# Kernel tuning notes

Hardware: AMD Instinct MI355X
Metric: run time of the kernel (lower is better)

## Reference

```python
import jax, jax.numpy as jnp
import numpy as np

EMBED_DIM = 1024
NUM_HEADS = 16
HEAD_DIM = EMBED_DIM // NUM_HEADS


def setup_inputs() -> dict:
    key = jax.random.key(0)
    k1, k2, k3, k4 = jax.random.split(key, 4)
    B, N, C = 4, 4096, EMBED_DIM
    x = jax.random.normal(k1, (B, N, C), dtype=jnp.float32)
    scale = 1.0 / np.sqrt(C)
    W_qkv = jax.random.normal(k2, (C, 3 * C), dtype=jnp.float32) * scale
    W_out = jax.random.normal(k3, (C, C), dtype=jnp.float32) * scale
    b_out = jax.random.normal(k4, (C,), dtype=jnp.float32) * 0.01
    return {"x": x, "W_qkv": W_qkv, "W_out": W_out, "b_out": b_out}


def reference(x, W_qkv, W_out, b_out):
    B, N, C = x.shape
    H, D = NUM_HEADS, HEAD_DIM
    qkv = (x @ W_qkv).reshape(B, N, 3, H, D)
    qkv = jnp.transpose(qkv, (2, 0, 3, 1, 4))  # (3, B, H, N, D)
    q, k, v = qkv[0], qkv[1], qkv[2]
    q = jax.nn.elu(q) + 1.0
    k = jax.nn.elu(k) + 1.0
    kv = jnp.einsum('bhnd,bhne->bhde', k, v)          # (B,H,D,D)
    num = jnp.einsum('bhnd,bhde->bhne', q, kv)        # (B,H,N,D)
    normalizer = jnp.einsum('bhnd,bhd->bhn', q, k.sum(axis=2))
    out = num / (normalizer[..., None] + 1e-6)
    out = jnp.transpose(out, (0, 2, 1, 3)).reshape(B, N, C)
    return out @ W_out + b_out
```

## Files before the change

kernel.cpp:

```cpp
#include <hip/hip_runtime.h>
#include <hip/hip_bf16.h>

using bf16x8 = __bf16 __attribute__((ext_vector_type(8)));
using f32x4  = float  __attribute__((ext_vector_type(4)));
using u16x8  = unsigned short __attribute__((ext_vector_type(8)));
using u16x4  = unsigned short __attribute__((ext_vector_type(4)));

__device__ __forceinline__ unsigned short f2bf(float f) {
  unsigned u = __builtin_bit_cast(unsigned, f);
  u += 0x7fffu + ((u >> 16) & 1u);
  return (unsigned short)(u >> 16);
}
__device__ __forceinline__ float bf2f(unsigned short h) {
  return __builtin_bit_cast(float, (unsigned)h << 16);
}

__device__ __forceinline__ void gload16(const void* g, void* l) {
  __builtin_amdgcn_global_load_lds(
      (const __attribute__((address_space(1))) void*)g,
      (__attribute__((address_space(3))) void*)l, 16, 0, 0);
}

__device__ __forceinline__ void barrier_raw() {
  asm volatile("" ::: "memory");
  __builtin_amdgcn_s_barrier();
  asm volatile("" ::: "memory");
}
#define VMC4() asm volatile("s_waitcnt vmcnt(4)" ::: "memory")
#define VMC0() asm volatile("s_waitcnt vmcnt(0)" ::: "memory")
#define SGB(mask, n) __builtin_amdgcn_sched_group_barrier(mask, n, 0)

__global__ __launch_bounds__(256) void conv_f32_bf16(const float* __restrict__ in,
                                                     unsigned short* __restrict__ out, int n) {
  int stride = gridDim.x * 256 * 4;
  for (int i = (blockIdx.x * 256 + threadIdx.x) * 4; i < n; i += stride) {
    float4 v = *reinterpret_cast<const float4*>(in + i);
    u16x4 o = { f2bf(v.x), f2bf(v.y), f2bf(v.z), f2bf(v.w) };
    *reinterpret_cast<u16x4*>(out + i) = o;
  }
}

__global__ __launch_bounds__(256) void transpose_f32_bf16(const float* __restrict__ in,
                                                          unsigned short* __restrict__ out,
                                                          int R, int C) {
  __shared__ float t[64][65];
  int c0 = blockIdx.x * 64, r0 = blockIdx.y * 64;
  int lx = threadIdx.x & 63, ly = threadIdx.x >> 6;
#pragma unroll
  for (int i = 0; i < 16; ++i) {
    int r = ly * 16 + i;
    t[r][lx] = in[(size_t)(r0 + r) * C + c0 + lx];
  }
  __syncthreads();
#pragma unroll
  for (int i = 0; i < 16; ++i) {
    int c = ly * 16 + i;
    out[(size_t)(c0 + c) * R + r0 + lx] = f2bf(t[lx][c]);
  }
}

__device__ __forceinline__ void gemm256_mainloop(
    const unsigned short* __restrict__ A, const unsigned short* __restrict__ Bt,
    int brow, int bcol, char* lds, f32x4 (&acc)[8][4]) {
  constexpr int NT = 16;
  const int tid  = threadIdx.x;
  const int lane = tid & 63;
  const int w    = tid >> 6;
  const int wr   = w >> 2, wc = w & 3;
  const int lr   = lane & 15, kg = lane >> 4;

  const int o0 = tid * 16;
  const int p0 = o0 ^ (((o0 >> 7) & 7) << 4);
  const int off0 = (p0 >> 7) * 2048 + (p0 & 127);
  const int wq = w << 10;

  const int xr  = (lr & 7) << 4;
  const int ck0 = (kg * 16) ^ xr;
  const int aoff = wr * 16384 + lr * 128;
  const int boff = 32768 + (wc >> 1) * 16384 + (wc & 1) * 8192 + lr * 128;

  const char* rA00 = lds + aoff + ck0;
  const char* rA01 = lds + aoff + (ck0 ^ 64);
  const char* rA10 = rA00 + 65536;
  const char* rA11 = rA01 + 65536;
  const char* rB00 = lds + boff + ck0;
  const char* rB01 = lds + boff + (ck0 ^ 64);
  const char* rB10 = rB00 + 65536;
  const char* rB11 = rB01 + 65536;

  const char* gA0 = (const char*)(A  + (size_t)brow * 1024) + off0;
  const char* gA1 = (const char*)(A  + (size_t)(brow + 128) * 1024) + off0;
  const char* gB0 = (const char*)(Bt + (size_t)bcol * 1024) + off0;
  const char* gB1 = (const char*)(Bt + (size_t)(bcol + 128) * 1024) + off0;

  auto STG = [&](const char*& g, int region) {
    gload16(g, lds + region + wq);
    gload16(g + 131072, lds + region + 8192 + wq);
    g += 128;
  };

  bf16x8 aQ[4][2], aR[4][2], bL0[2][2], bL1[2][2], bH[2][2];

  auto READ_A = [&](bf16x8 (&dst)[4][2], const char* pk0, const char* pk1, int mb) {
#pragma unroll
    for (int m = 0; m < 4; ++m) {
      dst[m][0] = __builtin_bit_cast(bf16x8, *(const u16x8*)(pk0 + (mb + m) * 2048));
      dst[m][1] = __builtin_bit_cast(bf16x8, *(const u16x8*)(pk1 + (mb + m) * 2048));
    }
  };
  auto READ_B = [&](bf16x8 (&dst)[2][2], const char* pk0, const char* pk1, int nb) {
#pragma unroll
    for (int n = 0; n < 2; ++n) {
      dst[n][0] = __builtin_bit_cast(bf16x8, *(const u16x8*)(pk0 + (nb + n) * 2048));
      dst[n][1] = __builtin_bit_cast(bf16x8, *(const u16x8*)(pk1 + (nb + n) * 2048));
    }
  };
  auto MFMA_Q = [&](int mb, int nb, bf16x8 (&Af)[4][2], bf16x8 (&Bf)[2][2]) {
#pragma unroll
    for (int kk = 0; kk < 2; ++kk)
#pragma unroll
      for (int m = 0; m < 4; ++m)
#pragma unroll
        for (int n = 0; n < 2; ++n)
          acc[mb + m][nb + n] =
              __builtin_amdgcn_mfma_f32_16x16x32_bf16(Af[m][kk], Bf[n][kk], acc[mb + m][nb + n], 0, 0, 0);
  };
  auto INTERLEAVE_P123 = [&]() {
#pragma unroll
    for (int s = 0; s < 12; ++s) { SGB(0x100, 1); SGB(0x8, 4); }
  };

  STG(gB0, 32768); STG(gB1, 49152);
  STG(gA0, 0);     STG(gA1, 16384);
  STG(gB0, 65536 + 32768); STG(gB1, 65536 + 49152);
  VMC4();
  barrier_raw();
  READ_A(aQ, rA00, rA01, 0);
  READ_B(bL0, rB00, rB01, 0);
  __builtin_amdgcn_s_setprio(1);

  for (int t = 0; t < NT; t += 2) {
    if (t + 1 < NT) { STG(gA0, 65536); STG(gA1, 65536 + 16384); }
    READ_B(bH, rB00, rB01, 2);
    MFMA_Q(0, 0, aQ, bL0);
    READ_A(aR, rA00, rA01, 4);
    MFMA_Q(0, 2, aQ, bH);
    MFMA_Q(4, 2, aR, bH);
    INTERLEAVE_P123();
    __builtin_amdgcn_s_setprio(0);
    barrier_raw();
    if (t + 2 < NT) {
      STG(gB0, 32768); STG(gB1, 49152);
      VMC4();
    } else if (t + 1 < NT) {
      VMC0();
    }
    barrier_raw();
    __builtin_amdgcn_s_setprio(1);
    if (t + 1 < NT) { READ_A(aQ, rA10, rA11, 0); READ_B(bL1, rB10, rB11, 0); }
    MFMA_Q(4, 0, aR, bL0);

    if (t + 1 < NT) {
      if (t + 2 < NT) { STG(gA0, 0); STG(gA1, 16384); }
      READ_B(bH, rB10, rB11, 2);
      MFMA_Q(0, 0, aQ, bL1);
      READ_A(aR, rA10, rA11, 4);
      MFMA_Q(0, 2, aQ, bH);
      MFMA_Q(4, 2, aR, bH);
      INTERLEAVE_P123();
      __builtin_amdgcn_s_setprio(0);
      barrier_raw();
      if (t + 3 < NT) {
        STG(gB0, 65536 + 32768); STG(gB1, 65536 + 49152);
        VMC4();
      } else if (t + 2 < NT) {
        VMC0();
      }
      barrier_raw();
      __builtin_amdgcn_s_setprio(1);
      if (t + 2 < NT) { READ_A(aQ, rA00, rA01, 0); READ_B(bL0, rB00, rB01, 0); }
      MFMA_Q(4, 0, aR, bL1);
    }
  }
  __builtin_amdgcn_s_setprio(0);
}

__global__ __launch_bounds__(512, 2) void gemm_qkv(
    const unsigned short* __restrict__ xbf, const unsigned short* __restrict__ wt,
    unsigned short* __restrict__ q, unsigned short* __restrict__ k, unsigned short* __restrict__ v) {
  __shared__ __align__(16) char lds[131072];
  f32x4 acc[8][4] = {};
  const int bid = blockIdx.x;
  const int r = bid & 7, i = bid >> 3;
  const int tm = r * 8 + (i & 7);
  const int tn = i >> 3;
  const int brow = tm * 256, bcol = tn * 256;
  gemm256_mainloop(xbf, wt, brow, bcol, lds, acc);

  const int lane = threadIdx.x & 63, w = threadIdx.x >> 6;
  const int wr = w >> 2, wc = w & 3;
  const int lr = lane & 15, kg = lane >> 4;
#pragma unroll
  for (int m = 0; m < 8; ++m)
#pragma unroll
    for (int n = 0; n < 4; ++n)
#pragma unroll
      for (int rr = 0; rr < 4; ++rr) {
        int grow = brow + wr * 128 + m * 16 + kg * 4 + rr;
        int gcol = bcol + wc * 64 + n * 16 + lr;
        float val = acc[m][n][rr];
        int tt = gcol >> 10;
        int h = (gcol >> 6) & 15;
        int d = gcol & 63;
        int b = grow >> 12, s = grow & 4095;
        size_t idx = ((size_t)(b * 16 + h) * 4096 + s) * 64 + d;
        if (tt < 2) {
          val = val > 0.f ? val + 1.f : __expf(val);
          (tt == 0 ? q : k)[idx] = f2bf(val);
        } else {
          v[idx] = f2bf(val);
        }
      }
}

__global__ __launch_bounds__(512, 2) void gemm_out(
    const unsigned short* __restrict__ attn, const unsigned short* __restrict__ wt,
    const float* __restrict__ bias, float* __restrict__ out) {
  __shared__ __align__(16) char lds[131072];
  f32x4 acc[8][4] = {};
  const int bid = blockIdx.x;
  const int r = bid & 7, i = bid >> 3;
  const int tm = r * 8 + (i & 7);
  const int tn = i >> 3;
  const int brow = tm * 256, bcol = tn * 256;
  gemm256_mainloop(attn, wt, brow, bcol, lds, acc);

  const int lane = threadIdx.x & 63, w = threadIdx.x >> 6;
  const int wr = w >> 2, wc = w & 3;
  const int lr = lane & 15, kg = lane >> 4;
#pragma unroll
  for (int m = 0; m < 8; ++m)
#pragma unroll
    for (int n = 0; n < 4; ++n)
#pragma unroll
      for (int rr = 0; rr < 4; ++rr) {
        int grow = brow + wr * 128 + m * 16 + kg * 4 + rr;
        int gcol = bcol + wc * 64 + n * 16 + lr;
        out[(size_t)grow * 1024 + gcol] = acc[m][n][rr] + bias[gcol];
      }
}

__global__ __launch_bounds__(256) void kv_kernel(
    const unsigned short* __restrict__ k, const unsigned short* __restrict__ v,
    float* __restrict__ kv, float* __restrict__ ksum) {
  const int bid = blockIdx.x;
  const int bh = bid >> 3, chunk = bid & 7;
  const unsigned short* kb = k + (size_t)bh * 4096 * 64 + chunk * 512 * 64;
  const unsigned short* vb = v + (size_t)bh * 4096 * 64 + chunk * 512 * 64;
  __shared__ unsigned short ks[64 * 64];
  __shared__ unsigned short vs[64 * 64];
  const int tid = threadIdx.x;
  const int ty = tid >> 4, tx = tid & 15;
  float acc[4][4] = {};
  float ksacc[4] = {};
  for (int t = 0; t < 8; ++t) {
    const unsigned short* ksrc = kb + t * 4096;
    const unsigned short* vsrc = vb + t * 4096;
    *reinterpret_cast<u16x8*>(&ks[tid * 8])        = *reinterpret_cast<const u16x8*>(ksrc + tid * 8);
    *reinterpret_cast<u16x8*>(&ks[2048 + tid * 8]) = *reinterpret_cast<const u16x8*>(ksrc + 2048 + tid * 8);
    *reinterpret_cast<u16x8*>(&vs[tid * 8])        = *reinterpret_cast<const u16x8*>(vsrc + tid * 8);
    *reinterpret_cast<u16x8*>(&vs[2048 + tid * 8]) = *reinterpret_cast<const u16x8*>(vsrc + 2048 + tid * 8);
    __syncthreads();
#pragma unroll 4
    for (int nn = 0; nn < 64; ++nn) {
      u16x4 ku = *reinterpret_cast<const u16x4*>(&ks[nn * 64 + ty * 4]);
      u16x4 vu = *reinterpret_cast<const u16x4*>(&vs[nn * 64 + tx * 4]);
      float kd[4], ve[4];
#pragma unroll
      for (int i = 0; i < 4; ++i) { kd[i] = bf2f(ku[i]); ve[i] = bf2f(vu[i]); }
#pragma unroll
      for (int i = 0; i < 4; ++i) ksacc[i] += kd[i];
#pragma unroll
      for (int i = 0; i < 4; ++i)
#pragma unroll
        for (int j = 0; j < 4; ++j) acc[i][j] += kd[i] * ve[j];
    }
    __syncthreads();
  }
  float* kvb = kv + (size_t)bh * 4096;
#pragma unroll
  for (int i = 0; i < 4; ++i)
#pragma unroll
    for (int j = 0; j < 4; ++j)
      atomicAdd(&kvb[(tx * 4 + j) * 64 + ty * 4 + i], acc[i][j]);
  if (tx == 0) {
#pragma unroll
    for (int i = 0; i < 4; ++i) atomicAdd(&ksum[bh * 64 + ty * 4 + i], ksacc[i]);
  }
}

__global__ __launch_bounds__(256) void num_kernel(
    const unsigned short* __restrict__ q, const float* __restrict__ kv,
    const float* __restrict__ ksum, unsigned short* __restrict__ attn) {
  const int bid = blockIdx.x;
  const int bh = bid >> 6, sblk = bid & 63;
  const int b = bh >> 4, h = bh & 15;
  __shared__ unsigned short kvs[64 * 72];
  __shared__ float ksum_s[64];
  __shared__ float norm_s[64];
  const int tid = threadIdx.x;
  const float* kvb = kv + (size_t)bh * 4096;
#pragma unroll
  for (int r = 0; r < 4; ++r) {
    int e = r * 1024 + tid * 4;
    float4 f = *reinterpret_cast<const float4*>(&kvb[e]);
    int row = e >> 6, col = e & 63;
    u16x4 o = { f2bf(f.x), f2bf(f.y), f2bf(f.z), f2bf(f.w) };
    *reinterpret_cast<u16x4*>(&kvs[row * 72 + col]) = o;
  }
  if (tid < 16) {
    float4 f = *reinterpret_cast<const float4*>(&ksum[bh * 64 + tid * 4]);
    ksum_s[tid * 4 + 0] = f.x; ksum_s[tid * 4 + 1] = f.y;
    ksum_s[tid * 4 + 2] = f.z; ksum_s[tid * 4 + 3] = f.w;
  }
  __syncthreads();

  const int lane = tid & 63, w = tid >> 6;
  const int lr = lane & 15, kg = lane >> 4;
  const int s0 = sblk * 64 + w * 16;
  const unsigned short* qrow = q + ((size_t)bh * 4096 + s0 + lr) * 64 + kg * 8;
  u16x8 a0u = *reinterpret_cast<const u16x8*>(qrow);
  u16x8 a1u = *reinterpret_cast<const u16x8*>(qrow + 32);
  bf16x8 a0 = __builtin_bit_cast(bf16x8, a0u);
  bf16x8 a1 = __builtin_bit_cast(bf16x8, a1u);

  float p = 0.f;
#pragma unroll
  for (int j = 0; j < 8; ++j) {
    p += bf2f(a0u[j]) * ksum_s[kg * 8 + j];
    p += bf2f(a1u[j]) * ksum_s[32 + kg * 8 + j];
  }
  p += __shfl_xor(p, 16);
  p += __shfl_xor(p, 32);
  if (kg == 0) norm_s[w * 16 + lr] = p;

  f32x4 accs[4];
#pragma unroll
  for (int jf = 0; jf < 4; ++jf) {
    u16x8 b0u = *reinterpret_cast<const u16x8*>(&kvs[(jf * 16 + lr) * 72 + kg * 8]);
    u16x8 b1u = *reinterpret_cast<const u16x8*>(&kvs[(jf * 16 + lr) * 72 + 32 + kg * 8]);
    f32x4 c = {0.f, 0.f, 0.f, 0.f};
    c = __builtin_amdgcn_mfma_f32_16x16x32_bf16(a0, __builtin_bit_cast(bf16x8, b0u), c, 0, 0, 0);
    c = __builtin_amdgcn_mfma_f32_16x16x32_bf16(a1, __builtin_bit_cast(bf16x8, b1u), c, 0, 0, 0);
    accs[jf] = c;
  }
  float dn[4];
#pragma unroll
  for (int r = 0; r < 4; ++r) dn[r] = norm_s[w * 16 + kg * 4 + r] + 1e-6f;

  unsigned short* ab = attn + (size_t)b * 4096 * 1024 + h * 64;
#pragma unroll
  for (int jf = 0; jf < 4; ++jf)
#pragma unroll
    for (int r = 0; r < 4; ++r) {
      int s = s0 + kg * 4 + r;
      int e2 = jf * 16 + lr;
      ab[(size_t)s * 1024 + e2] = f2bf(accs[jf][r] / dn[r]);
    }
}

extern "C" void kernel_launch(void* const* d_in, const int* in_sizes, int n_in,
                              void* d_out, int out_size, void* d_ws, size_t ws_size,
                              hipStream_t stream) {
  const float* x     = (const float*)d_in[0];
  const float* W_qkv = (const float*)d_in[1];
  const float* W_out = (const float*)d_in[2];
  const float* b_out = (const float*)d_in[3];
  float* out = (float*)d_out;

  unsigned short* xbf   = (unsigned short*)d_ws;
  unsigned short* attnb = xbf;
  unsigned short* wqkvT = xbf + 16777216;
  unsigned short* woutT = wqkvT + 3145728;
  unsigned short* qb    = woutT + 1048576;
  unsigned short* kb    = qb + 16777216;
  unsigned short* vb    = kb + 16777216;
  float* kvw            = (float*)(vb + 16777216);
  float* ksumw          = kvw + 262144;

  conv_f32_bf16<<<2048, 256, 0, stream>>>(x, xbf, 16777216);
  transpose_f32_bf16<<<dim3(48, 16), 256, 0, stream>>>(W_qkv, wqkvT, 1024, 3072);
  transpose_f32_bf16<<<dim3(16, 16), 256, 0, stream>>>(W_out, woutT, 1024, 1024);
  hipMemsetAsync(kvw, 0, (262144 + 4096) * sizeof(float), stream);
  gemm_qkv<<<768, 512, 0, stream>>>(xbf, wqkvT, qb, kb, vb);
  kv_kernel<<<512, 256, 0, stream>>>(kb, vb, kvw, ksumw);
  num_kernel<<<4096, 256, 0, stream>>>(qb, kvw, ksumw, attnb);
  gemm_out<<<256, 512, 0, stream>>>(attnb, woutT, b_out, out);
}
```

Before: 264.2 us.

## Restructure GEMM mainloop into ping-pong wave-group schedule with slot barriers

Replaces the hand-interleaved double-buffered mainloop with a KSTEP routine in which two wave groups (waves 0-3 and 4-7) run staggered phases, separated by barriers, so one group issues MFMAs while the other reads LDS. Each step issues all global-to-LDS loads for the next tile at once and waits for them with vmcnt(0). The MFMA blocks get raised priority and the scheduler is pinned with sched_barrier. The aim is better overlap of LDS reads and matrix math across waves. In exchange there are more barriers per step and the global loads are waited on fully rather than partially, which could expose memory latency.

```diff
diff --git a/kernel.cpp b/kernel.cpp
--- a/kernel.cpp
+++ b/kernel.cpp
@@ -21,14 +21,14 @@
       (__attribute__((address_space(3))) void*)l, 16, 0, 0);
 }
 
-__device__ __forceinline__ void barrier_raw() {
+__device__ __forceinline__ void slot_barrier() {
+  __builtin_amdgcn_sched_barrier(0);
   asm volatile("" ::: "memory");
   __builtin_amdgcn_s_barrier();
   asm volatile("" ::: "memory");
-}
-#define VMC4() asm volatile("s_waitcnt vmcnt(4)" ::: "memory")
+  __builtin_amdgcn_sched_barrier(0);
+}
 #define VMC0() asm volatile("s_waitcnt vmcnt(0)" ::: "memory")
-#define SGB(mask, n) __builtin_amdgcn_sched_group_barrier(mask, n, 0)
 
 __global__ __launch_bounds__(256) void conv_f32_bf16(const float* __restrict__ in,
                                                      unsigned short* __restrict__ out, int n) {
@@ -66,6 +66,7 @@
   const int tid  = threadIdx.x;
   const int lane = tid & 63;
   const int w    = tid >> 6;
+  const bool g0  = (w < 4);
   const int wr   = w >> 2, wc = w & 3;
   const int lr   = lane & 15, kg = lane >> 4;
 
@@ -99,7 +100,7 @@
     g += 128;
   };
 
-  bf16x8 aQ[4][2], aR[4][2], bL0[2][2], bL1[2][2], bH[2][2];
+  bf16x8 aQ[4][2], aR[4][2], bL[2][2], bH[2][2];
 
   auto READ_A = [&](bf16x8 (&dst)[4][2], const char* pk0, const char* pk1, int mb) {
 #pragma unroll
@@ -116,6 +117,7 @@
     }
   };
   auto MFMA_Q = [&](int mb, int nb, bf16x8 (&Af)[4][2], bf16x8 (&Bf)[2][2]) {
+    __builtin_amdgcn_s_setprio(1);
 #pragma unroll
     for (int kk = 0; kk < 2; ++kk)
 #pragma unroll
@@ -124,65 +126,67 @@
         for (int n = 0; n < 2; ++n)
           acc[mb + m][nb + n] =
               __builtin_amdgcn_mfma_f32_16x16x32_bf16(Af[m][kk], Bf[n][kk], acc[mb + m][nb + n], 0, 0, 0);
+    __builtin_amdgcn_s_setprio(0);
   };
-  auto INTERLEAVE_P123 = [&]() {
-#pragma unroll
-    for (int s = 0; s < 12; ++s) { SGB(0x100, 1); SGB(0x8, 4); }
+
+  auto KSTEP = [&](int t, const char* cA0, const char* cA1,
+                   const char* cB0, const char* cB1, int nbase) {
+    const bool notfirst = (t > 0);
+    const bool notlast  = (t + 1 < NT);
+    if (g0) {
+      if (notfirst) MFMA_Q(4, 0, aR, bL);
+      READ_A(aQ, cA0, cA1, 0);
+      READ_B(bL, cB0, cB1, 0);
+    } else {
+      if (notfirst) MFMA_Q(4, 2, aR, bH);
+    }
+    if (notlast) {
+      STG(gA0, nbase); STG(gA1, nbase + 16384);
+      STG(gB0, nbase + 32768); STG(gB1, nbase + 49152);
+    }
+    slot_barrier();
+    if (g0) {
+      MFMA_Q(0, 0, aQ, bL);
+      READ_B(bH, cB0, cB1, 2);
+    } else {
+      if (notfirst) MFMA_Q(4, 0, aR, bL);
+      READ_A(aQ, cA0, cA1, 0);
+      READ_B(bL, cB0, cB1, 0);
+    }
+    slot_barrier();
+    if (g0) {
+      MFMA_Q(0, 2, aQ, bH);
+      READ_A(aR, cA0, cA1, 4);
+    } else {
+      MFMA_Q(0, 0, aQ, bL);
+      READ_B(bH, cB0, cB1, 2);
+    }
+    slot_barrier();
+    if (g0) {
+      MFMA_Q(4, 2, aR, bH);
+    } else {
+      MFMA_Q(0, 2, aQ, bH);
+      READ_A(aR, cA0, cA1, 4);
+    }
+    if (notlast) VMC0();
+    slot_barrier();
   };
 
-  STG(gB0, 32768); STG(gB1, 49152);
-  STG(gA0, 0);     STG(gA1, 16384);
-  STG(gB0, 65536 + 32768); STG(gB1, 65536 + 49152);
-  VMC4();
-  barrier_raw();
-  READ_A(aQ, rA00, rA01, 0);
-  READ_B(bL0, rB00, rB01, 0);
-  __builtin_amdgcn_s_setprio(1);
+  STG(gA0, 0); STG(gA1, 16384); STG(gB0, 32768); STG(gB1, 49152);
+  VMC0();
+  slot_barrier();
 
   for (int t = 0; t < NT; t += 2) {
-    if (t + 1 < NT) { STG(gA0, 65536); STG(gA1, 65536 + 16384); }
-    READ_B(bH, rB00, rB01, 2);
-    MFMA_Q(0, 0, aQ, bL0);
-    READ_A(aR, rA00, rA01, 4);
-    MFMA_Q(0, 2, aQ, bH);
+    KSTEP(t,     rA00, rA01, rB00, rB01, 65536);
+    KSTEP(t + 1, rA10, rA11, rB10, rB11, 0);
+  }
+
+  if (g0) {
+    MFMA_Q(4, 0, aR, bL);
+  } else {
     MFMA_Q(4, 2, aR, bH);
-    INTERLEAVE_P123();
-    __builtin_amdgcn_s_setprio(0);
-    barrier_raw();
-    if (t + 2 < NT) {
-      STG(gB0, 32768); STG(gB1, 49152);
-      VMC4();
-    } else if (t + 1 < NT) {
-      VMC0();
-    }
-    barrier_raw();
-    __builtin_amdgcn_s_setprio(1);
-    if (t + 1 < NT) { READ_A(aQ, rA10, rA11, 0); READ_B(bL1, rB10, rB11, 0); }
-    MFMA_Q(4, 0, aR, bL0);
-
-    if (t + 1 < NT) {
-      if (t + 2 < NT) { STG(gA0, 0); STG(gA1, 16384); }
-      READ_B(bH, rB10, rB11, 2);
-      MFMA_Q(0, 0, aQ, bL1);
-      READ_A(aR, rA10, rA11, 4);
-      MFMA_Q(0, 2, aQ, bH);
-      MFMA_Q(4, 2, aR, bH);
-      INTERLEAVE_P123();
-      __builtin_amdgcn_s_setprio(0);
-      barrier_raw();
-      if (t + 3 < NT) {
-        STG(gB0, 65536 + 32768); STG(gB1, 65536 + 49152);
-        VMC4();
-      } else if (t + 2 < NT) {
-        VMC0();
-      }
-      barrier_raw();
-      __builtin_amdgcn_s_setprio(1);
-      if (t + 2 < NT) { READ_A(aQ, rA00, rA01, 0); READ_B(bL0, rB00, rB01, 0); }
-      MFMA_Q(4, 0, aR, bL1);
-    }
-  }
-  __builtin_amdgcn_s_setprio(0);
+    MFMA_Q(4, 0, aR, bL);
+  }
 }
 
 __global__ __launch_bounds__(512, 2) void gemm_qkv(
```

Measured after the change: 413.3 us. +56.4%, slower.

## Load GEMM B operand directly from global into registers, halve LDS footprint

Applied to the files above, without the earlier changes.

The shared GEMM mainloop no longer stages the B (weight) tile through LDS. Each wave loads its B fragments straight from global memory into registers, and LDS now holds only the double-buffered A tile, so the allocation drops from 128KB to 64KB. The aims are to remove LDS traffic and a barrier per stage and to allow more blocks per CU. The costs are redundant global reads of B across the wave rows, uncoalesced 16-byte strided loads, and dropping the sched_group_barrier interleaving, so the vmcnt(4) accounting now mixes register and LDS loads.

```diff
diff --git a/kernel.cpp b/kernel.cpp
--- a/kernel.cpp
+++ b/kernel.cpp
@@ -27,8 +27,6 @@
   asm volatile("" ::: "memory");
 }
 #define VMC4() asm volatile("s_waitcnt vmcnt(4)" ::: "memory")
-#define VMC0() asm volatile("s_waitcnt vmcnt(0)" ::: "memory")
-#define SGB(mask, n) __builtin_amdgcn_sched_group_barrier(mask, n, 0)
 
 __global__ __launch_bounds__(256) void conv_f32_bf16(const float* __restrict__ in,
                                                      unsigned short* __restrict__ out, int n) {
@@ -77,21 +75,19 @@
   const int xr  = (lr & 7) << 4;
   const int ck0 = (kg * 16) ^ xr;
   const int aoff = wr * 16384 + lr * 128;
-  const int boff = 32768 + (wc >> 1) * 16384 + (wc & 1) * 8192 + lr * 128;
 
   const char* rA00 = lds + aoff + ck0;
   const char* rA01 = lds + aoff + (ck0 ^ 64);
-  const char* rA10 = rA00 + 65536;
-  const char* rA11 = rA01 + 65536;
-  const char* rB00 = lds + boff + ck0;
-  const char* rB01 = lds + boff + (ck0 ^ 64);
-  const char* rB10 = rB00 + 65536;
-  const char* rB11 = rB01 + 65536;
-
-  const char* gA0 = (const char*)(A  + (size_t)brow * 1024) + off0;
-  const char* gA1 = (const char*)(A  + (size_t)(brow + 128) * 1024) + off0;
-  const char* gB0 = (const char*)(Bt + (size_t)bcol * 1024) + off0;
-  const char* gB1 = (const char*)(Bt + (size_t)(bcol + 128) * 1024) + off0;
+  const char* rA10 = rA00 + 32768;
+  const char* rA11 = rA01 + 32768;
+
+  const char* gA0 = (const char*)(A + (size_t)brow * 1024) + off0;
+  const char* gA1 = (const char*)(A + (size_t)(brow + 128) * 1024) + off0;
+
+  const char* gB[4];
+#pragma unroll
+  for (int n = 0; n < 4; ++n)
+    gB[n] = (const char*)(Bt + (size_t)(bcol + wc * 64 + n * 16 + lr) * 1024) + kg * 16;
 
   auto STG = [&](const char*& g, int region) {
     gload16(g, lds + region + wq);
@@ -108,14 +104,15 @@
       dst[m][1] = __builtin_bit_cast(bf16x8, *(const u16x8*)(pk1 + (mb + m) * 2048));
     }
   };
-  auto READ_B = [&](bf16x8 (&dst)[2][2], const char* pk0, const char* pk1, int nb) {
+  auto GLOAD_B = [&](bf16x8 (&dst)[2][2], int nb, int tbytes) {
 #pragma unroll
     for (int n = 0; n < 2; ++n) {
-      dst[n][0] = __builtin_bit_cast(bf16x8, *(const u16x8*)(pk0 + (nb + n) * 2048));
-      dst[n][1] = __builtin_bit_cast(bf16x8, *(const u16x8*)(pk1 + (nb + n) * 2048));
+      dst[n][0] = __builtin_bit_cast(bf16x8, *(const u16x8*)(gB[nb + n] + tbytes));
+      dst[n][1] = __builtin_bit_cast(bf16x8, *(const u16x8*)(gB[nb + n] + tbytes + 64));
     }
   };
   auto MFMA_Q = [&](int mb, int nb, bf16x8 (&Af)[4][2], bf16x8 (&Bf)[2][2]) {
+    __builtin_amdgcn_s_setprio(1);
 #pragma unroll
     for (int kk = 0; kk < 2; ++kk)
 #pragma unroll
@@ -124,71 +121,48 @@
         for (int n = 0; n < 2; ++n)
           acc[mb + m][nb + n] =
               __builtin_amdgcn_mfma_f32_16x16x32_bf16(Af[m][kk], Bf[n][kk], acc[mb + m][nb + n], 0, 0, 0);
+    __builtin_amdgcn_s_setprio(0);
   };
-  auto INTERLEAVE_P123 = [&]() {
-#pragma unroll
-    for (int s = 0; s < 12; ++s) { SGB(0x100, 1); SGB(0x8, 4); }
-  };
-
-  STG(gB0, 32768); STG(gB1, 49152);
-  STG(gA0, 0);     STG(gA1, 16384);
-  STG(gB0, 65536 + 32768); STG(gB1, 65536 + 49152);
+
+  STG(gA0, 0); STG(gA1, 16384);
+  GLOAD_B(bL0, 0, 0);
   VMC4();
   barrier_raw();
   READ_A(aQ, rA00, rA01, 0);
-  READ_B(bL0, rB00, rB01, 0);
-  __builtin_amdgcn_s_setprio(1);
 
   for (int t = 0; t < NT; t += 2) {
-    if (t + 1 < NT) { STG(gA0, 65536); STG(gA1, 65536 + 16384); }
-    READ_B(bH, rB00, rB01, 2);
+    GLOAD_B(bH, 2, t << 7);
+    if (t + 1 < NT) { STG(gA0, 32768); STG(gA1, 49152); }
     MFMA_Q(0, 0, aQ, bL0);
     READ_A(aR, rA00, rA01, 4);
     MFMA_Q(0, 2, aQ, bH);
+    if (t + 1 < NT) GLOAD_B(bL1, 0, (t + 1) << 7);
     MFMA_Q(4, 2, aR, bH);
-    INTERLEAVE_P123();
-    __builtin_amdgcn_s_setprio(0);
+    if (t + 1 < NT) VMC4();
     barrier_raw();
-    if (t + 2 < NT) {
-      STG(gB0, 32768); STG(gB1, 49152);
-      VMC4();
-    } else if (t + 1 < NT) {
-      VMC0();
-    }
-    barrier_raw();
-    __builtin_amdgcn_s_setprio(1);
-    if (t + 1 < NT) { READ_A(aQ, rA10, rA11, 0); READ_B(bL1, rB10, rB11, 0); }
+    if (t + 1 < NT) READ_A(aQ, rA10, rA11, 0);
     MFMA_Q(4, 0, aR, bL0);
 
     if (t + 1 < NT) {
+      GLOAD_B(bH, 2, (t + 1) << 7);
       if (t + 2 < NT) { STG(gA0, 0); STG(gA1, 16384); }
-      READ_B(bH, rB10, rB11, 2);
       MFMA_Q(0, 0, aQ, bL1);
       READ_A(aR, rA10, rA11, 4);
       MFMA_Q(0, 2, aQ, bH);
+      if (t + 2 < NT) GLOAD_B(bL0, 0, (t + 2) << 7);
       MFMA_Q(4, 2, aR, bH);
-      INTERLEAVE_P123();
-      __builtin_amdgcn_s_setprio(0);
+      if (t + 2 < NT) VMC4();
       barrier_raw();
-      if (t + 3 < NT) {
-        STG(gB0, 65536 + 32768); STG(gB1, 65536 + 49152);
-        VMC4();
-      } else if (t + 2 < NT) {
-        VMC0();
-      }
-      barrier_raw();
-      __builtin_amdgcn_s_setprio(1);
-      if (t + 2 < NT) { READ_A(aQ, rA00, rA01, 0); READ_B(bL0, rB00, rB01, 0); }
+      if (t + 2 < NT) READ_A(aQ, rA00, rA01, 0);
       MFMA_Q(4, 0, aR, bL1);
     }
   }
-  __builtin_amdgcn_s_setprio(0);
 }
 
 __global__ __launch_bounds__(512, 2) void gemm_qkv(
     const unsigned short* __restrict__ xbf, const unsigned short* __restrict__ wt,
     unsigned short* __restrict__ q, unsigned short* __restrict__ k, unsigned short* __restrict__ v) {
-  __shared__ __align__(16) char lds[131072];
+  __shared__ __align__(16) char lds[65536];
   f32x4 acc[8][4] = {};
   const int bid = blockIdx.x;
   const int r = bid & 7, i = bid >> 3;
@@ -226,7 +200,7 @@
 __global__ __launch_bounds__(512, 2) void gemm_out(
     const unsigned short* __restrict__ attn, const unsigned short* __restrict__ wt,
     const float* __restrict__ bias, float* __restrict__ out) {
-  __shared__ __align__(16) char lds[131072];
+  __shared__ __align__(16) char lds[65536];
   f32x4 acc[8][4] = {};
   const int bid = blockIdx.x;
   const int r = bid & 7, i = bid >> 3;
```

After: 418.1 us. 1.58x slower.
